# Kernel tuning notes

Hardware: AMD Instinct MI355X
Metric: run time of the kernel (lower is better)

The kernel has to match this reference:

```python
import jax, jax.numpy as jnp
import numpy as np
from jax import lax

DN = ('NCHW', 'OIHW', 'NCHW')
BN_EPS = 1e-5


def _avg_pool(x, k, stride):
    # PyTorch AvgPool2d with count_include_pad=True: divide by k*k always
    p = k // 2
    s = lax.reduce_window(x, 0.0, lax.add, (1, 1, k, k), (1, 1, stride, stride),
                          [(0, 0), (0, 0), (p, p), (p, p)])
    return s / float(k * k)


def setup_inputs() -> dict:
    key = jax.random.key(0)
    k0, k1, k2 = jax.random.split(key, 3)
    x = jax.random.normal(k0, (8, 3, 1024, 1024), jnp.float32)
    weight = jax.random.normal(k1, (1, 5), jnp.float32)          # nn.Parameter(1,5)
    conv_w = jax.random.normal(k2, (5, 3, 7, 7), jnp.float32) * 0.05
    bn_gamma = jnp.ones((5,), jnp.float32)
    bn_beta = jnp.zeros((5,), jnp.float32)
    bn_mean = jnp.zeros((5,), jnp.float32)
    bn_var = jnp.ones((5,), jnp.float32)
    return {"x": x, "weight": weight, "conv_w": conv_w,
            "bn_gamma": bn_gamma, "bn_beta": bn_beta,
            "bn_mean": bn_mean, "bn_var": bn_var}


def reference(x, weight, conv_w, bn_gamma, bn_beta, bn_mean, bn_var):
    # stage 1: 3x3 avgpool stride 2
    x = _avg_pool(x, 3, 2)                                  # [b,3,512,512]
    image_a = jnp.mean(x, axis=1, keepdims=True)            # [b,1,512,512]

    # attention branch: Conv(3->5,k7,s2,p3) + BN(eval) -> spatial mean -> tanh
    wa = lax.conv_general_dilated(x, conv_w, (2, 2), [(3, 3), (3, 3)],
                                  dimension_numbers=DN)     # [b,5,256,256]
    wa = (wa - bn_mean[None, :, None, None]) * (bn_gamma[None, :, None, None] /
          jnp.sqrt(bn_var[None, :, None, None] + BN_EPS)) + bn_beta[None, :, None, None]
    weight_att = jnp.tanh(jnp.mean(wa, axis=(2, 3)))        # [b,5]

    # Gaussian-Laplacian kernel from learned scalar GL
    GL = weight[0, 0]
    a1 = GL * 4.0
    a2 = -a1 / 8.0
    a3 = -a1 / 16.0
    ker = jnp.zeros((1, 1, 5, 5), jnp.float32)
    for r, c in [(0, 2), (1, 1), (1, 3), (2, 0), (2, 4), (3, 1), (3, 3), (4, 2)]:
        ker = ker.at[0, 0, r, c].set(a3)
    for r, c in [(1, 2), (2, 1), (2, 3), (3, 2)]:
        ker = ker.at[0, 0, r, c].set(a2)
    ker = ker.at[0, 0, 2, 2].set(a1)

    x_GL = lax.conv_general_dilated(image_a, ker, (1, 1), [(2, 2), (2, 2)],
                                    dimension_numbers=DN)   # [b,1,512,512]
    x_GL = jnp.abs(x_GL)
    x_GL = jnp.where(x_GL < 1e-6, 0.0, x_GL)                # zero tiny values (relu is no-op after abs)

    b, c, h, w = x_GL.shape
    t = x_GL.reshape(b, 1, h * w)                           # [b,1,N]
    x_GL_max = jnp.max(t, axis=-1)                          # [b,1]
    pos = t > 0
    all_sum = jnp.sum(pos, axis=-1)                         # [b,1]

    # 101 cubic-spaced bin edges in [0,10]
    xv = jnp.asarray(10.0 * (np.arange(101, dtype=np.float64) / 100.0) ** 3, jnp.float32)  # [101]
    sub_sum = jnp.sum(pos & (t <= xv[None, :, None]), axis=-1)  # [b,101]
    percentage = sub_sum.astype(jnp.float32) / all_sum.astype(jnp.float32)  # [b,101]

    # per-sample target percentiles (sorted)
    ps = jnp.stack([0.2 + 0.05 * weight_att[:, 1],
                    0.4 + 0.05 * weight_att[:, 2],
                    0.6 + 0.05 * weight_att[:, 3],
                    0.8 + 0.05 * weight_att[:, 4]])         # [4,b]
    thr_pct = jnp.sort(ps, axis=0).T                        # [b,4]

    z = jnp.abs(percentage[:, None, :] - thr_pct[:, :, None])  # [b,4,101]
    closest = jnp.argmin(z, axis=-1)                        # [b,4]
    threshold = xv[closest]                                 # [b,4]

    t_min = jnp.concatenate([jnp.zeros_like(x_GL_max), threshold], axis=-1)[:, :, None]  # [b,5,1]
    t_max = jnp.concatenate([threshold, x_GL_max], axis=-1)[:, :, None]                  # [b,5,1]
    mask = ((t > t_min) & (t <= t_max)).astype(jnp.float32).reshape(b, 5, h, w)

    # multi-stage 9x9 avg pooling
    m = _avg_pool(mask, 9, 1)
    m = _avg_pool(m, 9, 1)
    m = _avg_pool(m, 9, 2)                                  # [b,5,h//2,w//2]
    m = m.reshape(b, 5, -1)
    mn = jnp.min(m, axis=2, keepdims=True)
    mx = jnp.max(m, axis=2, keepdims=True)
    norm = (m - mn) / (mx - mn)
    return norm.reshape(b, 5, h // 2, w // 2)
```

## Files before the change

kernel.cpp:

```cpp
#include <hip/hip_runtime.h>
#include <math.h>

#pragma clang fp contract(off)

#define B 8
#define SP2 262144
#define SP3 65536

#define POOLF  4194304
#define MASKQF 6291456
#define TRIHF  10485760
#define TAILF  20971520

__global__ void k1_pool3(const float* __restrict__ x, double* __restrict__ imga,
                         double* __restrict__ rcs) {
    __shared__ double redE[2][3][128], redO[2][3][128];
    __shared__ double edge[2][3][5];
    int blk = (blockIdx.x & 7) * 256 + (blockIdx.x >> 3);
    int tid = threadIdx.x;
    int q = tid & 127;
    int r = tid >> 7;
    int rowIdx = blk * 2 + r;
    int yo = rowIdx & 511;
    int b  = rowIdx >> 9;
    int xb = 8 * q;
    double pv[3][4];
    for (int c = 0; c < 3; ++c) {
        const float* p = x + ((size_t)(b * 3 + c)) * 1048576;
        double s0 = 0.0, s1 = 0.0, s2 = 0.0, s3 = 0.0;
        #pragma unroll
        for (int dy = 0; dy < 3; ++dy) {
            int iy = 2 * yo - 1 + dy;
            if ((unsigned)iy >= 1024u) continue;
            const float* row = p + (size_t)iy * 1024 + xb;
            float4 fM = *(const float4*)row;
            float4 fR = *(const float4*)(row + 4);
            float  vm1 = (q > 0) ? row[-1] : 0.f;
            s0 += (double)vm1  + (double)fM.x + (double)fM.y;
            s1 += (double)fM.y + (double)fM.z + (double)fM.w;
            s2 += (double)fM.w + (double)fR.x + (double)fR.y;
            s3 += (double)fR.y + (double)fR.z + (double)fR.w;
        }
        pv[c][0] = s0 * (1.0 / 9.0); pv[c][1] = s1 * (1.0 / 9.0);
        pv[c][2] = s2 * (1.0 / 9.0); pv[c][3] = s3 * (1.0 / 9.0);
        redE[r][c][q] = pv[c][0] + pv[c][2];
        redO[r][c][q] = pv[c][1] + pv[c][3];
        if (q == 0)   { edge[r][c][0] = pv[c][0]; edge[r][c][1] = pv[c][1]; }
        if (q == 127) { edge[r][c][2] = pv[c][1]; edge[r][c][3] = pv[c][2]; edge[r][c][4] = pv[c][3]; }
    }
    double* ia = imga + (size_t)b * SP2 + yo * 512 + 4 * q;
    #pragma unroll
    for (int k = 0; k < 4; ++k)
        ia[k] = ((pv[0][k] + pv[1][k]) + pv[2][k]) * (1.0 / 3.0);
    __syncthreads();
    for (int s = 64; s > 0; s >>= 1) {
        if (q < s) {
            #pragma unroll
            for (int c = 0; c < 3; ++c) {
                redE[r][c][q] += redE[r][c][q + s];
                redO[r][c][q] += redO[r][c][q + s];
            }
        }
        __syncthreads();
    }
    if (q < 21) {
        int c = q / 7, kx = q - c * 7;
        double E = redE[r][c][0], O = redO[r][c][0];
        double val;
        switch (kx) {
            case 0: val = O - edge[r][c][2] - edge[r][c][4]; break;
            case 1: val = E - edge[r][c][3]; break;
            case 2: val = O - edge[r][c][4]; break;
            case 3: val = E; break;
            case 4: val = O; break;
            case 5: val = E - edge[r][c][0]; break;
            default: val = O - edge[r][c][1]; break;
        }
        rcs[((size_t)(b * 3 + c) * 512 + yo) * 7 + kx] = val;
    }
}

__global__ void kS(const double* __restrict__ rcs, double* __restrict__ S) {
    int blk = blockIdx.x;
    int ky = blk % 7;
    int bc = blk / 7;
    int t = threadIdx.x;
    double v[7] = {0, 0, 0, 0, 0, 0, 0};
    int iy = 2 * t + ky - 3;
    if ((unsigned)iy < 512u) {
        const double* p = rcs + ((size_t)bc * 512 + iy) * 7;
        #pragma unroll
        for (int kx = 0; kx < 7; ++kx) v[kx] = p[kx];
    }
    __shared__ double red[7][256];
    #pragma unroll
    for (int kx = 0; kx < 7; ++kx) red[kx][t] = v[kx];
    __syncthreads();
    for (int s = 128; s > 0; s >>= 1) {
        if (t < s) {
            #pragma unroll
            for (int kx = 0; kx < 7; ++kx)
                red[kx][t] += red[kx][t + s];
        }
        __syncthreads();
    }
    if (t < 7) S[(size_t)blk * 7 + t] = red[t][0];
}

__global__ void k3_gl(const double* __restrict__ imga, const float* __restrict__ weight,
                      uchar4* __restrict__ codes) {
    __shared__ double xv[101];
    for (int i = threadIdx.x; i < 101; i += 256) {
        double d = (double)i / 100.0;
        xv[i] = (double)(float)(10.0 * d * d * d);
    }
    __syncthreads();
    int idx = blockIdx.x * 256 + threadIdx.x;
    int xo = idx & 511;
    int yo = (idx >> 9) & 511;
    int b  = idx >> 18;
    const double* im = imga + (size_t)b * SP2;
    double GL = (double)weight[0];
    double a1 = GL * 4.0, a2 = -a1 / 8.0, a3 = -a1 / 16.0;
    auto g = [&](int y, int x) -> double {
        if ((unsigned)y >= 512u || (unsigned)x >= 512u) return 0.0;
        return im[y * 512 + x];
    };
    double v = a1 * g(yo, xo)
             + a2 * (g(yo - 1, xo) + g(yo, xo - 1) + g(yo, xo + 1) + g(yo + 1, xo))
             + a3 * (g(yo - 2, xo) + g(yo - 1, xo - 1) + g(yo - 1, xo + 1) + g(yo, xo - 2)
                   + g(yo, xo + 2) + g(yo + 1, xo - 1) + g(yo + 1, xo + 1) + g(yo + 2, xo));
    double t = fabs(v);
    const double EPS = 6e-7;
    int cM;
    if (t < 1e-6) cM = 255;
    else if (t > xv[100]) cM = 101;
    else {
        int lo = 0, hi = 100;
        while (lo < hi) { int mid = (lo + hi) >> 1; if (t <= xv[mid]) hi = mid; else lo = mid + 1; }
        cM = lo;
    }
    double ua = t - EPS;
    int cA;
    if (ua < 1e-6) cA = 255;
    else if (ua > xv[100]) cA = 101;
    else {
        int k = (cM == 101) ? 100 : ((cM == 255) ? 100 : cM);
        while (k > 0 && ua <= xv[k - 1]) --k;
        cA = k;
    }
    double ub = t + EPS;
    int cB;
    if (ub < 1e-6) cB = 255;
    else if (ub > xv[100]) cB = 101;
    else {
        int k = (cM == 255) ? 0 : ((cM == 101) ? 100 : cM);
        while (k < 100 && ub > xv[k]) ++k;
        cB = k;
    }
    codes[idx] = make_uchar4((unsigned char)cM, (unsigned char)cA, (unsigned char)cB, 0);
}

__global__ void k4_hist(const uchar4* __restrict__ codes, int* __restrict__ ghist) {
    int b = blockIdx.y;
    __shared__ int h[102];
    for (int i = threadIdx.x; i < 102; i += 256) h[i] = 0;
    __syncthreads();
    const uint4* cb = (const uint4*)(codes + (size_t)b * SP2);
    for (int p = blockIdx.x * 256 + threadIdx.x; p < SP2 / 4; p += 64 * 256) {
        uint4 v = cb[p];
        int c0 = v.x & 255, c1 = v.y & 255, c2 = v.z & 255, c3 = v.w & 255;
        if (c0 != 255) atomicAdd(&h[c0], 1);
        if (c1 != 255) atomicAdd(&h[c1], 1);
        if (c2 != 255) atomicAdd(&h[c2], 1);
        if (c3 != 255) atomicAdd(&h[c3], 1);
    }
    __syncthreads();
    for (int i = threadIdx.x; i < 102; i += 256)
        if (h[i]) atomicAdd(&ghist[b * 102 + i], h[i]);
}

__global__ void k5_thr(const double* __restrict__ S, const float* __restrict__ convw,
                       const int* __restrict__ ghist,
                       const float* __restrict__ bn_gamma, const float* __restrict__ bn_beta,
                       const float* __restrict__ bn_mean, const float* __restrict__ bn_var,
                       int* __restrict__ thrLo, int* __restrict__ thrHi) {
    int b = blockIdx.x;
    int t = threadIdx.x;
    __shared__ int    hS[102];
    __shared__ int    cumI[101];
    __shared__ double pct[101];
    __shared__ double ps[4];
    __shared__ int    allS;
    if (t < 102) hS[t] = ghist[b * 102 + t];
    if (t < 4) {
        int o = t + 1;
        double acc = 0.0;
        #pragma unroll 7
        for (int tap = 0; tap < 147; ++tap) {
            int c = tap / 49;
            int k = tap - c * 49;
            int ky = k / 7, kx = k - ky * 7;
            acc += (double)convw[o * 147 + tap] * S[(((size_t)(b * 3 + c)) * 7 + ky) * 7 + kx];
        }
        double m = acc / 65536.0;
        double scale = (double)bn_gamma[o] / sqrt((double)bn_var[o] + 1e-5);
        double val = (m - (double)bn_mean[o]) * scale + (double)bn_beta[o];
        const double base[4] = {0.2, 0.4, 0.6, 0.8};
        ps[t] = base[t] + 0.05 * tanh(val);
    }
    __syncthreads();
    if (t == 0) {
        int all = 0;
        for (int k = 0; k < 102; ++k) all += hS[k];
        allS = all;
        int cum = 0;
        for (int k = 0; k < 101; ++k) { cum += hS[k]; cumI[k] = cum; }
        for (int i = 0; i < 4; ++i)
            for (int j = i + 1; j < 4; ++j)
                if (ps[j] < ps[i]) { double tp = ps[i]; ps[i] = ps[j]; ps[j] = tp; }
    }
    __syncthreads();
    double alld = (double)allS;
    if (t < 101) pct[t] = (double)cumI[t] / alld;
    __syncthreads();
    if (t < 4) {
        const double EPS_TIE = 1.2e-7;
        double target = ps[t];
        double best = 1e300; int bi = 0;
        for (int k = 0; k < 101; ++k) {
            double z = fabs(pct[k] - target);
            if (z < best) { best = z; bi = k; }
        }
        int lo = bi, hi = bi;
        for (int k = 0; k < 101; ++k) {
            double z = fabs(pct[k] - target);
            if (z <= best + EPS_TIE) { if (k < lo) lo = k; if (k > hi) hi = k; }
        }
        int cnt = cumI[hi] - cumI[lo];
        if (cnt > 2) { lo = bi; hi = bi; }
        thrLo[b * 4 + t] = lo;
        thrHi[b * 4 + t] = hi;
    }
}

__global__ void k6_mask(const uchar4* __restrict__ codes, const int* __restrict__ thrLo,
                        const int* __restrict__ thrHi, unsigned char* __restrict__ mq) {
    int idx4 = blockIdx.x * 256 + threadIdx.x;
    int b  = idx4 >> 16;
    int sp0 = (idx4 & 65535) * 4;
    const uchar4* cb = codes + (size_t)b * SP2 + sp0;
    uchar4 cd[4] = {cb[0], cb[1], cb[2], cb[3]};
    const int* tL = thrLo + b * 4;
    const int* tH = thrHi + b * 4;
    int t0L = tL[0], t1L = tL[1], t2L = tL[2], t3L = tL[3];
    int t0H = tH[0], t1H = tH[1], t2H = tH[2], t3H = tH[3];
    unsigned char wv[5][4];
    #pragma unroll
    for (int px = 0; px < 4; ++px) {
        int w0 = 0, w1 = 0, w2 = 0, w3 = 0, w4 = 0;
        int cand[2] = {cd[px].y, cd[px].z};
        #pragma unroll
        for (int ci = 0; ci < 2; ++ci) {
            int c = cand[ci];
            if (c == 255) continue;
            if (c <= t0L) ++w0; else if (c <= t1L) ++w1; else if (c <= t2L) ++w2;
            else if (c <= t3L) ++w3; else ++w4;
            if (c <= t0H) ++w0; else if (c <= t1H) ++w1; else if (c <= t2H) ++w2;
            else if (c <= t3H) ++w3; else ++w4;
        }
        wv[0][px] = (unsigned char)w0; wv[1][px] = (unsigned char)w1;
        wv[2][px] = (unsigned char)w2; wv[3][px] = (unsigned char)w3;
        wv[4][px] = (unsigned char)w4;
    }
    unsigned char* mb = mq + (size_t)b * 5 * SP2 + sp0;
    #pragma unroll
    for (int pl = 0; pl < 5; ++pl)
        *(uchar4*)(mb + (size_t)pl * SP2) = make_uchar4(wv[pl][0], wv[pl][1], wv[pl][2], wv[pl][3]);
}

__global__ void __launch_bounds__(512) k7f(const unsigned char* __restrict__ mq,
                                           float* __restrict__ out,
                                           float* __restrict__ pmn, float* __restrict__ pmx) {
    __shared__ unsigned short shH[39][512];
    __shared__ unsigned short shB[31][512];
    __shared__ float smn[512], smx[512];
    unsigned short (*shT)[512] = shH;
    int (*shD)[256] = (int (*)[256])shB;

    int blk = (blockIdx.x & 7) * 160 + (blockIdx.x >> 3);
    int g  = blk & 31;
    int ch = blk >> 5;
    int y0 = g * 8;
    int tid = threadIdx.x;
    int lane = tid & 63;
    int rsel = tid >> 6;

    for (int it = 0; it < 5; ++it) {
        int rl = 8 * it + rsel;
        if (rl >= 39) break;
        int gr = 2 * y0 - 12 + rl;
        int x0 = lane * 8;
        uint4 pk = make_uint4(0u, 0u, 0u, 0u);
        if ((unsigned)gr < 512u) {
            const uint2* r8 = (const uint2*)(mq + (size_t)ch * SP2 + (size_t)gr * 512);
            uint2 cL = (lane > 0)  ? r8[lane - 1] : make_uint2(0u, 0u);
            uint2 cM = r8[lane];
            uint2 cR = (lane < 63) ? r8[lane + 1] : make_uint2(0u, 0u);
            int v[24];
            auto unpack = [](uint2 c, int* dst) {
                dst[0] = c.x & 255; dst[1] = (c.x >> 8) & 255; dst[2] = (c.x >> 16) & 255; dst[3] = (c.x >> 24) & 255;
                dst[4] = c.y & 255; dst[5] = (c.y >> 8) & 255; dst[6] = (c.y >> 16) & 255; dst[7] = (c.y >> 24) & 255;
            };
            unpack(cL, v); unpack(cM, v + 8); unpack(cR, v + 16);
            int bx[16];
            int s = 0;
            #pragma unroll
            for (int i = 0; i < 9; ++i) s += v[i];
            bx[0] = s;
            #pragma unroll
            for (int k = 1; k < 16; ++k) { s += v[k + 8] - v[k - 1]; bx[k] = s; }
            if (lane == 0)  { bx[0] = 0; bx[1] = 0; bx[2] = 0; bx[3] = 0; }
            if (lane == 63) { bx[12] = 0; bx[13] = 0; bx[14] = 0; bx[15] = 0; }
            int t = 0;
            #pragma unroll
            for (int i = 0; i < 9; ++i) t += bx[i];
            unsigned short o[8];
            o[0] = (unsigned short)t;
            #pragma unroll
            for (int i = 1; i < 8; ++i) { t += bx[i + 8] - bx[i - 1]; o[i] = (unsigned short)t; }
            pk.x = (unsigned)o[0] | ((unsigned)o[1] << 16);
            pk.y = (unsigned)o[2] | ((unsigned)o[3] << 16);
            pk.z = (unsigned)o[4] | ((unsigned)o[5] << 16);
            pk.w = (unsigned)o[6] | ((unsigned)o[7] << 16);
        }
        *(uint4*)&shH[rl][x0] = pk;
    }
    __syncthreads();

    {
        int x = tid;
        int s = 0;
        #pragma unroll
        for (int i = 0; i < 9; ++i) s += (int)shH[i][x];
        int j0 = 2 * y0 - 8;
        unsigned short bv[31];
        bv[0] = (unsigned short)(((unsigned)j0 < 512u) ? s : 0);
        #pragma unroll
        for (int jl = 1; jl < 31; ++jl) {
            s += (int)shH[jl + 8][x] - (int)shH[jl - 1][x];
            int j = j0 + jl;
            bv[jl] = (unsigned short)(((unsigned)j < 512u) ? s : 0);
        }
        #pragma unroll
        for (int jl = 0; jl < 31; ++jl) shB[jl][x] = bv[jl];
    }
    __syncthreads();

    {
        int x = tid;
        int s = 0;
        #pragma unroll
        for (int i = 0; i < 9; ++i) s += (int)shB[i][x];
        unsigned short tv[23];
        tv[0] = (unsigned short)s;
        #pragma unroll
        for (int rl = 1; rl < 23; ++rl) {
            s += (int)shB[rl + 8][x] - (int)shB[rl - 1][x];
            tv[rl] = (unsigned short)s;
        }
        #pragma unroll
        for (int rl = 0; rl < 23; ++rl) shT[rl][x] = tv[rl];
    }
    __syncthreads();

    for (int it = 0; it < 3; ++it) {
        int rl = 8 * it + rsel;
        if (rl >= 23) break;
        int gr = 2 * y0 - 4 + rl;
        int ox0 = lane * 4;
        int o0 = 0, o1 = 0, o2 = 0, o3 = 0;
        if ((unsigned)gr < 512u) {
            int v[15];
            #pragma unroll
            for (int i = 0; i < 15; ++i) {
                int ix = 2 * ox0 - 4 + i;
                v[i] = ((unsigned)ix < 512u) ? (int)shT[rl][ix] : 0;
            }
            int s = 0;
            #pragma unroll
            for (int i = 0; i < 9; ++i) s += v[i];
            o0 = s;
            s += v[9] + v[10] - v[0] - v[1];   o1 = s;
            s += v[11] + v[12] - v[2] - v[3];  o2 = s;
            s += v[13] + v[14] - v[4] - v[5];  o3 = s;
        }
        shD[rl][ox0] = o0; shD[rl][ox0 + 1] = o1; shD[rl][ox0 + 2] = o2; shD[rl][ox0 + 3] = o3;
    }
    __syncthreads();

    int x = tid & 255;
    int dy0 = (tid >> 8) * 4;
    float lmn = 3.4e38f, lmx = -3.4e38f;
    float* op = out + (size_t)ch * SP3 + (size_t)y0 * 256 + x;
    #pragma unroll
    for (int k = 0; k < 4; ++k) {
        int dy = dy0 + k;
        int s = 0;
        #pragma unroll
        for (int d = 0; d < 9; ++d) s += shD[2 * dy + d][x];
        float val = (float)s / 2125764.0f;
        op[(size_t)dy * 256] = val;
        lmn = fminf(lmn, val); lmx = fmaxf(lmx, val);
    }
    smn[tid] = lmn; smx[tid] = lmx;
    __syncthreads();
    for (int st = 256; st > 0; st >>= 1) {
        if (tid < st) {
            smn[tid] = fminf(smn[tid], smn[tid + st]);
            smx[tid] = fmaxf(smx[tid], smx[tid + st]);
        }
        __syncthreads();
    }
    if (tid == 0) { pmn[blk] = smn[0]; pmx[blk] = smx[0]; }
}

__global__ void k9_norm(float* __restrict__ o, const float* __restrict__ pmn,
                        const float* __restrict__ pmx) {
    __shared__ float sm[2];
    int idx = blockIdx.x * 256 + threadIdx.x;
    int ch = idx >> 16;
    int lane = threadIdx.x & 63;
    if (threadIdx.x < 64) {
        float v = (lane < 32) ? pmn[ch * 32 + lane] : pmx[ch * 32 + (lane - 32)];
        #pragma unroll
        for (int off = 16; off > 0; off >>= 1) {
            float u = __shfl_xor(v, off, 64);
            v = (lane < 32) ? fminf(v, u) : fmaxf(v, u);
        }
        if (lane == 0)  sm[0] = v;
        if (lane == 32) sm[1] = v;
    }
    __syncthreads();
    float a = sm[0];
    float bmax = sm[1];
    o[idx] = (o[idx] - a) / (bmax - a);
}

extern "C" void kernel_launch(void* const* d_in, const int* in_sizes, int n_in,
                              void* d_out, int out_size, void* d_ws, size_t ws_size,
                              hipStream_t stream) {
    const float* x      = (const float*)d_in[0];
    const float* weight = (const float*)d_in[1];
    const float* conv_w = (const float*)d_in[2];
    const float* bn_g   = (const float*)d_in[3];
    const float* bn_b   = (const float*)d_in[4];
    const float* bn_m   = (const float*)d_in[5];
    const float* bn_v   = (const float*)d_in[6];
    float* out = (float*)d_out;
    float* ws  = (float*)d_ws;

    double* imga   = (double*)ws;
    uchar4* codes  = (uchar4*)(ws + POOLF);
    unsigned char* maskq = (unsigned char*)(ws + MASKQF);
    double* rcs    = (double*)(ws + TRIHF);
    double* S       = (double*)(ws + TAILF);
    int*    thrLo   = (int*)(ws + TAILF + 2368);
    int*    thrHi   = thrLo + 32;
    int*    ghist   = thrHi + 32;
    float*  pmn     = (float*)(ghist + 816);
    float*  pmx     = pmn + 1280;

    hipMemsetAsync(ghist, 0, 816 * sizeof(int), stream);

    k1_pool3  <<<2048, 256, 0, stream>>>(x, imga, rcs);
    kS        <<<168, 256, 0, stream>>>(rcs, S);
    k3_gl     <<<8192, 256, 0, stream>>>(imga, weight, codes);
    k4_hist   <<<dim3(64, B), 256, 0, stream>>>(codes, ghist);
    k5_thr    <<<B, 128, 0, stream>>>(S, conv_w, ghist, bn_g, bn_b, bn_m, bn_v, thrLo, thrHi);
    k6_mask   <<<2048, 256, 0, stream>>>(codes, thrLo, thrHi, maskq);
    k7f       <<<1280, 512, 0, stream>>>(maskq, out, pmn, pmx);
    k9_norm   <<<10240, 256, 0, stream>>>(out, pmn, pmx);
}
```

Baseline: 118.6 us.

## Fuse Laplacian code generation with per-batch histogram accumulation

Merges the Gaussian-Laplacian/code kernel and the histogram kernel into one launch. Each block processes 4096 pixels of one batch image in a 16-iteration loop and accumulates the histogram in shared memory while producing codes. This removes a kernel launch and the re-read of the codes buffer. The cost is a much smaller grid (512 blocks), which lowers occupancy for latency hiding.

```diff
diff --git a/kernel.cpp b/kernel.cpp
--- a/kernel.cpp
+++ b/kernel.cpp
@@ -107,73 +107,63 @@
     if (t < 7) S[(size_t)blk * 7 + t] = red[t][0];
 }
 
-__global__ void k3_gl(const double* __restrict__ imga, const float* __restrict__ weight,
-                      uchar4* __restrict__ codes) {
+__global__ void k34_gl(const double* __restrict__ imga, const float* __restrict__ weight,
+                       uchar4* __restrict__ codes, int* __restrict__ ghist) {
     __shared__ double xv[101];
+    __shared__ int h[102];
     for (int i = threadIdx.x; i < 101; i += 256) {
         double d = (double)i / 100.0;
         xv[i] = (double)(float)(10.0 * d * d * d);
     }
-    __syncthreads();
-    int idx = blockIdx.x * 256 + threadIdx.x;
-    int xo = idx & 511;
-    int yo = (idx >> 9) & 511;
-    int b  = idx >> 18;
+    for (int i = threadIdx.x; i < 102; i += 256) h[i] = 0;
+    __syncthreads();
+    int b = blockIdx.y;
     const double* im = imga + (size_t)b * SP2;
     double GL = (double)weight[0];
     double a1 = GL * 4.0, a2 = -a1 / 8.0, a3 = -a1 / 16.0;
-    auto g = [&](int y, int x) -> double {
-        if ((unsigned)y >= 512u || (unsigned)x >= 512u) return 0.0;
-        return im[y * 512 + x];
-    };
-    double v = a1 * g(yo, xo)
-             + a2 * (g(yo - 1, xo) + g(yo, xo - 1) + g(yo, xo + 1) + g(yo + 1, xo))
-             + a3 * (g(yo - 2, xo) + g(yo - 1, xo - 1) + g(yo - 1, xo + 1) + g(yo, xo - 2)
-                   + g(yo, xo + 2) + g(yo + 1, xo - 1) + g(yo + 1, xo + 1) + g(yo + 2, xo));
-    double t = fabs(v);
     const double EPS = 6e-7;
-    int cM;
-    if (t < 1e-6) cM = 255;
-    else if (t > xv[100]) cM = 101;
-    else {
-        int lo = 0, hi = 100;
-        while (lo < hi) { int mid = (lo + hi) >> 1; if (t <= xv[mid]) hi = mid; else lo = mid + 1; }
-        cM = lo;
-    }
-    double ua = t - EPS;
-    int cA;
-    if (ua < 1e-6) cA = 255;
-    else if (ua > xv[100]) cA = 101;
-    else {
-        int k = (cM == 101) ? 100 : ((cM == 255) ? 100 : cM);
-        while (k > 0 && ua <= xv[k - 1]) --k;
-        cA = k;
-    }
-    double ub = t + EPS;
-    int cB;
-    if (ub < 1e-6) cB = 255;
-    else if (ub > xv[100]) cB = 101;
-    else {
-        int k = (cM == 255) ? 0 : ((cM == 101) ? 100 : cM);
-        while (k < 100 && ub > xv[k]) ++k;
-        cB = k;
-    }
-    codes[idx] = make_uchar4((unsigned char)cM, (unsigned char)cA, (unsigned char)cB, 0);
-}
-
-__global__ void k4_hist(const uchar4* __restrict__ codes, int* __restrict__ ghist) {
-    int b = blockIdx.y;
-    __shared__ int h[102];
-    for (int i = threadIdx.x; i < 102; i += 256) h[i] = 0;
-    __syncthreads();
-    const uint4* cb = (const uint4*)(codes + (size_t)b * SP2);
-    for (int p = blockIdx.x * 256 + threadIdx.x; p < SP2 / 4; p += 64 * 256) {
-        uint4 v = cb[p];
-        int c0 = v.x & 255, c1 = v.y & 255, c2 = v.z & 255, c3 = v.w & 255;
-        if (c0 != 255) atomicAdd(&h[c0], 1);
-        if (c1 != 255) atomicAdd(&h[c1], 1);
-        if (c2 != 255) atomicAdd(&h[c2], 1);
-        if (c3 != 255) atomicAdd(&h[c3], 1);
+    for (int i = 0; i < 16; ++i) {
+        int sp = blockIdx.x * 4096 + i * 256 + threadIdx.x;
+        int xo = sp & 511;
+        int yo = sp >> 9;
+        auto g = [&](int y, int x) -> double {
+            if ((unsigned)y >= 512u || (unsigned)x >= 512u) return 0.0;
+            return im[y * 512 + x];
+        };
+        double v = a1 * g(yo, xo)
+                 + a2 * (g(yo - 1, xo) + g(yo, xo - 1) + g(yo, xo + 1) + g(yo + 1, xo))
+                 + a3 * (g(yo - 2, xo) + g(yo - 1, xo - 1) + g(yo - 1, xo + 1) + g(yo, xo - 2)
+                       + g(yo, xo + 2) + g(yo + 1, xo - 1) + g(yo + 1, xo + 1) + g(yo + 2, xo));
+        double t = fabs(v);
+        int cM;
+        if (t < 1e-6) cM = 255;
+        else if (t > xv[100]) cM = 101;
+        else {
+            int lo = 0, hi = 100;
+            while (lo < hi) { int mid = (lo + hi) >> 1; if (t <= xv[mid]) hi = mid; else lo = mid + 1; }
+            cM = lo;
+        }
+        double ua = t - EPS;
+        int cA;
+        if (ua < 1e-6) cA = 255;
+        else if (ua > xv[100]) cA = 101;
+        else {
+            int k = (cM == 101) ? 100 : ((cM == 255) ? 100 : cM);
+            while (k > 0 && ua <= xv[k - 1]) --k;
+            cA = k;
+        }
+        double ub = t + EPS;
+        int cB;
+        if (ub < 1e-6) cB = 255;
+        else if (ub > xv[100]) cB = 101;
+        else {
+            int k = (cM == 255) ? 0 : ((cM == 101) ? 100 : cM);
+            while (k < 100 && ub > xv[k]) ++k;
+            cB = k;
+        }
+        codes[(size_t)b * SP2 + sp] = make_uchar4((unsigned char)cM, (unsigned char)cA,
+                                                  (unsigned char)cB, 0);
+        if (cM != 255) atomicAdd(&h[cM], 1);
     }
     __syncthreads();
     for (int i = threadIdx.x; i < 102; i += 256)
@@ -475,8 +465,7 @@
 
     k1_pool3  <<<2048, 256, 0, stream>>>(x, imga, rcs);
     kS        <<<168, 256, 0, stream>>>(rcs, S);
-    k3_gl     <<<8192, 256, 0, stream>>>(imga, weight, codes);
-    k4_hist   <<<dim3(64, B), 256, 0, stream>>>(codes, ghist);
+    k34_gl    <<<dim3(64, B), 256, 0, stream>>>(imga, weight, codes, ghist);
     k5_thr    <<<B, 128, 0, stream>>>(S, conv_w, ghist, bn_g, bn_b, bn_m, bn_v, thrLo, thrHi);
     k6_mask   <<<2048, 256, 0, stream>>>(codes, thrLo, thrHi, maskq);
     k7f       <<<1280, 512, 0, stream>>>(maskq, out, pmn, pmx);
```

After: 127.6 us. 1.08x slower.
